# Optimization experiments

Hardware: AMD Instinct MI355X
Metric: run time of the kernel (lower is better)

## Reference

```python
import jax, jax.numpy as jnp
import numpy as np

ALPHA = 0.01  # matches LineFinderLoss(alpha=0.01)


def setup_inputs() -> dict:
    key = jax.random.key(0)
    k1, k2 = jax.random.split(key)
    S = 4096  # square so N == M == S (required for the original code to run)
    # column 4 is used as a probability: log(c) and log(1-c) must be finite
    inp = jax.random.uniform(k1, (S, S), dtype=jnp.float32, minval=1e-4, maxval=1.0 - 1e-4)
    tgt = jax.random.uniform(k2, (S, S), dtype=jnp.float32)
    return {"input": inp, "target": tgt}


def reference(input, target):
    N = input.shape[1]
    M = target.shape[1]
    # pairwise MSE cost over the first two coordinates: cost[n,m] = mean((input[n,:2]-target[m,:2])^2)
    diff = input[:, None, 0:2] - target[None, :, 0:2]  # [N, M, 2]
    cost = jnp.mean(diff * diff, axis=-1)              # [N, M]
    # Hungarian on an NxN cost yields a full assignment; the original code sets
    # X[p,l]=1 for the OUTER PRODUCT of matched row/col index sets, so X == ones
    # deterministically (matching does not affect the output).
    X = jnp.ones((N, M), dtype=input.dtype)
    mse_full = jnp.mean((input - target) ** 2)  # self.mse(input, target), constant over (n,m)
    log_c = jnpp_log = jnp.log(input[:, 4])     # [N]
    log_1mc = jnp.log(1.0 - input[:, 4])        # [N]
    # sum_{n,m} X*(alpha*mse_full - log c_n) - (1-X)*log(1-c_n)
    term = X * (ALPHA * mse_full - log_c[:, None]) - (1.0 - X) * log_1mc[:, None]
    # torch mse_loss(input[:,3], target) broadcasts (S,) against (S,S): elem [i,j] = (input[j,3]-target[i,j])^2
    loss = jnp.sum(term) + jnp.mean((input[:, 3] - target) ** 2)
    return loss, cost
```

## Files before the change

kernel.cpp:

```cpp
#include <hip/hip_runtime.h>

#define SDIM 4096
#define ALPHA 0.01f
#define WS_ARR 32
#define RBLOCKS 2048
#define WS_PART (WS_ARR + 5 * SDIM)


__global__ void k_gather(const float* __restrict__ inp, const float* __restrict__ tgt,
                         float* __restrict__ ws) {
    __shared__ float sbuf[4];
    int n = blockIdx.x * blockDim.x + threadIdx.x;
    const float* row = inp + (size_t)n * SDIM;
    const float* trow = tgt + (size_t)n * SDIM;
    float* arr = ws + WS_ARR;

    float v0 = row[0], v1 = row[1], v3 = row[3], v4 = row[4];
    arr[n]            = v0;
    arr[SDIM + n]     = v1;
    arr[2 * SDIM + n] = v3;
    arr[3 * SDIM + n] = trow[0];
    arr[4 * SDIM + n] = trow[1];

    float lg = logf(v4);
    #pragma unroll
    for (int off = 32; off > 0; off >>= 1) lg += __shfl_down(lg, off);
    if ((threadIdx.x & 63) == 0) sbuf[threadIdx.x >> 6] = lg;
    __syncthreads();
    if (threadIdx.x == 0)
        ws[8 + blockIdx.x] = sbuf[0] + sbuf[1] + sbuf[2] + sbuf[3];
}

__global__ void k_cost(const float* __restrict__ ws, float* __restrict__ out) {
    const float* c0 = ws + WS_ARR;
    const float* c1 = c0 + SDIM;
    const float* t0 = c0 + 3 * SDIM;
    const float* t1 = c0 + 4 * SDIM;

    int n = blockIdx.y;
    float a0 = c0[n];
    float a1 = c1[n];
    int base = blockIdx.x * 1024;
    float* orow = out + 1 + (size_t)n * SDIM + base;
    int t = threadIdx.x;
    #pragma unroll
    for (int k = 0; k < 4; ++k) {
        int m = base + k * 256 + t;
        float d0 = a0 - t0[m];
        float d1 = a1 - t1[m];
        orow[k * 256 + t] = 0.5f * (d0 * d0 + d1 * d1);
    }
}

__global__ void k_reduce(const float* __restrict__ inp, const float* __restrict__ tgt,
                         float* __restrict__ ws) {
    __shared__ float s1[4], s2[4];
    const float* c3 = ws + WS_ARR + 2 * SDIM;

    const size_t nvec = (size_t)SDIM * SDIM / 4;
    float a1 = 0.0f, a2 = 0.0f;
    for (size_t v = (size_t)blockIdx.x * blockDim.x + threadIdx.x; v < nvec;
         v += (size_t)gridDim.x * blockDim.x) {
        size_t f = v * 4;
        float4 vi = *(const float4*)(inp + f);
        float4 vt = *(const float4*)(tgt + f);
        float4 vc = *(const float4*)(c3 + (int)(f & (SDIM - 1)));
        float d;
        d = vi.x - vt.x; a1 += d * d;
        d = vi.y - vt.y; a1 += d * d;
        d = vi.z - vt.z; a1 += d * d;
        d = vi.w - vt.w; a1 += d * d;
        d = vc.x - vt.x; a2 += d * d;
        d = vc.y - vt.y; a2 += d * d;
        d = vc.z - vt.z; a2 += d * d;
        d = vc.w - vt.w; a2 += d * d;
    }

    #pragma unroll
    for (int off = 32; off > 0; off >>= 1) {
        a1 += __shfl_down(a1, off);
        a2 += __shfl_down(a2, off);
    }
    int wave = threadIdx.x >> 6;
    if ((threadIdx.x & 63) == 0) { s1[wave] = a1; s2[wave] = a2; }
    __syncthreads();
    if (threadIdx.x == 0) {
        ws[WS_PART + blockIdx.x]           = s1[0] + s1[1] + s1[2] + s1[3];
        ws[WS_PART + RBLOCKS + blockIdx.x] = s2[0] + s2[1] + s2[2] + s2[3];
    }
}

__global__ void k_final(const float* __restrict__ ws, float* __restrict__ out) {
    __shared__ float s1[4], s2[4];
    float a1 = 0.0f, a2 = 0.0f;
    for (int i = threadIdx.x; i < RBLOCKS; i += 256) {
        a1 += ws[WS_PART + i];
        a2 += ws[WS_PART + RBLOCKS + i];
    }
    #pragma unroll
    for (int off = 32; off > 0; off >>= 1) {
        a1 += __shfl_down(a1, off);
        a2 += __shfl_down(a2, off);
    }
    int wave = threadIdx.x >> 6;
    if ((threadIdx.x & 63) == 0) { s1[wave] = a1; s2[wave] = a2; }
    __syncthreads();
    if (threadIdx.x == 0) {
        float sum_sq = s1[0] + s1[1] + s1[2] + s1[3];
        float sum3   = s2[0] + s2[1] + s2[2] + s2[3];
        float slog = 0.0f;
        #pragma unroll
        for (int i = 0; i < 16; ++i) slog += ws[8 + i];
        out[0] = ALPHA * sum_sq - (float)SDIM * slog
               + sum3 * (1.0f / ((float)SDIM * (float)SDIM));
    }
}

extern "C" void kernel_launch(void* const* d_in, const int* in_sizes, int n_in,
                              void* d_out, int out_size, void* d_ws, size_t ws_size,
                              hipStream_t stream) {
    const float* inp = (const float*)d_in[0];
    const float* tgt = (const float*)d_in[1];
    float* out = (float*)d_out;
    float* ws  = (float*)d_ws;

    k_gather<<<16, 256, 0, stream>>>(inp, tgt, ws);
    k_cost<<<dim3(4, 4096), 256, 0, stream>>>(ws, out);
    k_reduce<<<RBLOCKS, 256, 0, stream>>>(inp, tgt, ws);
    k_final<<<1, 256, 0, stream>>>(ws, out);
}
```

Before: 180.8 us.

## Fuse cost-matrix write and full reduction into one row-per-block kernel

Merges the cost-matrix kernel and the grid-stride reduction kernel into one kernel with one block per row. Each block loads its input and target rows as float4 for the two squared-error sums and also writes that row of the cost matrix. This removes a kernel launch and lets read and write traffic overlap within the same kernel. The per-block partial count rises to 4096, so the final reduction reads more values.

```diff
diff --git a/kernel.cpp b/kernel.cpp
--- a/kernel.cpp
+++ b/kernel.cpp
@@ -3,7 +3,6 @@
 #define SDIM 4096
 #define ALPHA 0.01f
 #define WS_ARR 32
-#define RBLOCKS 2048
 #define WS_PART (WS_ARR + 5 * SDIM)
 
 
@@ -31,49 +30,55 @@
         ws[8 + blockIdx.x] = sbuf[0] + sbuf[1] + sbuf[2] + sbuf[3];
 }
 
-__global__ void k_cost(const float* __restrict__ ws, float* __restrict__ out) {
+__global__ void __launch_bounds__(256) k_main(const float* __restrict__ inp,
+                                              const float* __restrict__ tgt,
+                                              const float* __restrict__ ws,
+                                              float* __restrict__ out,
+                                              float* __restrict__ wpart) {
+    __shared__ float s1[4], s2[4];
     const float* c0 = ws + WS_ARR;
     const float* c1 = c0 + SDIM;
+    const float* c3 = c0 + 2 * SDIM;
     const float* t0 = c0 + 3 * SDIM;
     const float* t1 = c0 + 4 * SDIM;
 
-    int n = blockIdx.y;
+    int n = blockIdx.x;
+    int t = threadIdx.x;
     float a0 = c0[n];
-    float a1 = c1[n];
-    int base = blockIdx.x * 1024;
-    float* orow = out + 1 + (size_t)n * SDIM + base;
-    int t = threadIdx.x;
+    float b0 = c1[n];
+
+    const float* irow = inp + (size_t)n * SDIM;
+    const float* trow = tgt + (size_t)n * SDIM;
+    float* orow = out + 1 + (size_t)n * SDIM;
+
+    float4 vi[4], vt[4], vc[4];
     #pragma unroll
     for (int k = 0; k < 4; ++k) {
-        int m = base + k * 256 + t;
-        float d0 = a0 - t0[m];
-        float d1 = a1 - t1[m];
-        orow[k * 256 + t] = 0.5f * (d0 * d0 + d1 * d1);
+        int col = (k * 256 + t) * 4;
+        vi[k] = *(const float4*)(irow + col);
+        vt[k] = *(const float4*)(trow + col);
+        vc[k] = *(const float4*)(c3 + col);
     }
-}
+    float a1 = 0.0f, a2 = 0.0f;
+    #pragma unroll
+    for (int k = 0; k < 4; ++k) {
+        float d;
+        d = vi[k].x - vt[k].x; a1 += d * d;
+        d = vi[k].y - vt[k].y; a1 += d * d;
+        d = vi[k].z - vt[k].z; a1 += d * d;
+        d = vi[k].w - vt[k].w; a1 += d * d;
+        d = vc[k].x - vt[k].x; a2 += d * d;
+        d = vc[k].y - vt[k].y; a2 += d * d;
+        d = vc[k].z - vt[k].z; a2 += d * d;
+        d = vc[k].w - vt[k].w; a2 += d * d;
+    }
 
-__global__ void k_reduce(const float* __restrict__ inp, const float* __restrict__ tgt,
-                         float* __restrict__ ws) {
-    __shared__ float s1[4], s2[4];
-    const float* c3 = ws + WS_ARR + 2 * SDIM;
-
-    const size_t nvec = (size_t)SDIM * SDIM / 4;
-    float a1 = 0.0f, a2 = 0.0f;
-    for (size_t v = (size_t)blockIdx.x * blockDim.x + threadIdx.x; v < nvec;
-         v += (size_t)gridDim.x * blockDim.x) {
-        size_t f = v * 4;
-        float4 vi = *(const float4*)(inp + f);
-        float4 vt = *(const float4*)(tgt + f);
-        float4 vc = *(const float4*)(c3 + (int)(f & (SDIM - 1)));
-        float d;
-        d = vi.x - vt.x; a1 += d * d;
-        d = vi.y - vt.y; a1 += d * d;
-        d = vi.z - vt.z; a1 += d * d;
-        d = vi.w - vt.w; a1 += d * d;
-        d = vc.x - vt.x; a2 += d * d;
-        d = vc.y - vt.y; a2 += d * d;
-        d = vc.z - vt.z; a2 += d * d;
-        d = vc.w - vt.w; a2 += d * d;
+    #pragma unroll
+    for (int k = 0; k < 16; ++k) {
+        int j = k * 256 + t;
+        float d0 = a0 - t0[j];
+        float d1 = b0 - t1[j];
+        orow[j] = 0.5f * (d0 * d0 + d1 * d1);
     }
 
     #pragma unroll
@@ -81,21 +86,22 @@
         a1 += __shfl_down(a1, off);
         a2 += __shfl_down(a2, off);
     }
-    int wave = threadIdx.x >> 6;
-    if ((threadIdx.x & 63) == 0) { s1[wave] = a1; s2[wave] = a2; }
+    int wave = t >> 6;
+    if ((t & 63) == 0) { s1[wave] = a1; s2[wave] = a2; }
     __syncthreads();
-    if (threadIdx.x == 0) {
-        ws[WS_PART + blockIdx.x]           = s1[0] + s1[1] + s1[2] + s1[3];
-        ws[WS_PART + RBLOCKS + blockIdx.x] = s2[0] + s2[1] + s2[2] + s2[3];
+    if (t == 0) {
+        wpart[n]        = s1[0] + s1[1] + s1[2] + s1[3];
+        wpart[SDIM + n] = s2[0] + s2[1] + s2[2] + s2[3];
     }
 }
 
 __global__ void k_final(const float* __restrict__ ws, float* __restrict__ out) {
     __shared__ float s1[4], s2[4];
     float a1 = 0.0f, a2 = 0.0f;
-    for (int i = threadIdx.x; i < RBLOCKS; i += 256) {
-        a1 += ws[WS_PART + i];
-        a2 += ws[WS_PART + RBLOCKS + i];
+    const float* wpart = ws + WS_PART;
+    for (int i = threadIdx.x; i < SDIM; i += 256) {
+        a1 += wpart[i];
+        a2 += wpart[SDIM + i];
     }
     #pragma unroll
     for (int off = 32; off > 0; off >>= 1) {
@@ -125,7 +131,6 @@
     float* ws  = (float*)d_ws;
 
     k_gather<<<16, 256, 0, stream>>>(inp, tgt, ws);
-    k_cost<<<dim3(4, 4096), 256, 0, stream>>>(ws, out);
-    k_reduce<<<RBLOCKS, 256, 0, stream>>>(inp, tgt, ws);
+    k_main<<<SDIM, 256, 0, stream>>>(inp, tgt, ws, out, ws + WS_PART);
     k_final<<<1, 256, 0, stream>>>(ws, out);
 }
```

Result: no change. 180.9 us (+0.0%).
